# Kernel tuning notes

Measured on AMD Instinct MI355X. Metric: run time of the kernel, lower is better.

Reference implementation:

```python
import jax, jax.numpy as jnp
import numpy as np

H_HEADS = 16
N_HID = 1024
D_K = N_HID // H_HEADS
EPS = 1e-6


def _linear(x, w, b):
    # torch nn.Linear: y = x @ W^T + b, W is [out, in]
    return jnp.einsum('bsi,oi->bso', x, w) + b


def _layernorm(x, a, b):
    # Faithful to custom LayerNorm: unbiased std (torch default) and (std + eps)
    mean = jnp.mean(x, axis=-1, keepdims=True)
    std = jnp.std(x, axis=-1, keepdims=True, ddof=1)
    return a * (x - mean) / (std + EPS) + b


def setup_inputs() -> dict:
    key = jax.random.key(0)
    ks = jax.random.split(key, 20)
    B, S, H = 4, 1024, N_HID
    s = 1.0 / np.sqrt(H)
    inp = {
        'x': jax.random.normal(ks[0], (B, S, H), dtype=jnp.float32),
        'mask': jax.random.randint(ks[1], (B, 1, 1, S), 0, 2, dtype=jnp.int32),
        'wq': jax.random.normal(ks[2], (H, H), dtype=jnp.float32) * s,
        'bq': jnp.zeros((H,), jnp.float32),
        'wk': jax.random.normal(ks[3], (H, H), dtype=jnp.float32) * s,
        'bk': jnp.zeros((H,), jnp.float32),
        'wv': jax.random.normal(ks[4], (H, H), dtype=jnp.float32) * s,
        'bv': jnp.zeros((H,), jnp.float32),
        'wo': jax.random.normal(ks[5], (H, H), dtype=jnp.float32) * s,
        'bo': jnp.zeros((H,), jnp.float32),
        'w1': jax.random.normal(ks[6], (2 * H, H), dtype=jnp.float32) * s,
        'b1': jnp.zeros((2 * H,), jnp.float32),
        'w2': jax.random.normal(ks[7], (H, 2 * H), dtype=jnp.float32) * (1.0 / np.sqrt(2 * H)),
        'b2': jnp.zeros((H,), jnp.float32),
        'g1': jnp.ones((H,), jnp.float32),
        'be1': jnp.zeros((H,), jnp.float32),
        'g2': jnp.ones((H,), jnp.float32),
        'be2': jnp.zeros((H,), jnp.float32),
    }
    return inp


def _forward(x, mask, wq, bq, wk, bk, wv, bv, wo, bo, w1, b1, w2, b2, g1, be1, g2, be2):
    B, S, H = x.shape
    # --- multi-head self-attention ---
    q = _linear(x, wq, bq).reshape(B, S, H_HEADS, D_K).transpose(0, 2, 1, 3)  # [B,h,S,dk]
    k = _linear(x, wk, bk).reshape(B, S, H_HEADS, D_K).transpose(0, 2, 1, 3)
    v = _linear(x, wv, bv).reshape(B, S, H_HEADS, D_K).transpose(0, 2, 1, 3)
    scores = jnp.einsum('bhqd,bhkd->bhqk', q, k) / np.sqrt(D_K)  # [B,h,S,S]
    scores = jnp.where(mask == 0, jnp.float32(-1e9), scores)
    p = jax.nn.softmax(scores, axis=-1)
    attn_out = jnp.einsum('bhqk,bhkd->bhqd', p, v)
    attn_out = attn_out.transpose(0, 2, 1, 3).reshape(B, S, H)
    attn_out = _linear(attn_out, wo, bo)
    # sublayer 0: residual + layernorm (dropout = identity at eval)
    x = _layernorm(x + attn_out, g1, be1)
    # --- positionwise FFN ---
    ff = _linear(jax.nn.relu(_linear(x, w1, b1)), w2, b2)
    # sublayer 1
    return _layernorm(x + ff, g2, be2)


def reference(x, mask, wq, bq, wk, bk, wv, bv, wo, bo, w1, b1, w2, b2, g1, be1, g2, be2):
    return _forward(x, mask, wq, bq, wk, bk, wv, bv, wo, bo, w1, b1, w2, b2, g1, be1, g2, be2)
```

## Files before the change

### kernel.cpp

```cpp
#include <hip/hip_runtime.h>

typedef __attribute__((ext_vector_type(8))) short short8;
typedef __attribute__((ext_vector_type(4))) float f32x4;
typedef __attribute__((ext_vector_type(4))) unsigned short us4;

#define LOG2E 1.4426950408889634f

__device__ __forceinline__ unsigned short f2bf(float f) {
  unsigned int u = __float_as_uint(f);
  u += 0x7FFFu + ((u >> 16) & 1u);
  return (unsigned short)(u >> 16);
}

__global__ __launch_bounds__(256) void cvt_all(
    const float* __restrict__ x, const float* __restrict__ wq, const float* __restrict__ wk,
    const float* __restrict__ wv, const float* __restrict__ wo, const float* __restrict__ w1,
    const float* __restrict__ w2,
    unsigned short* __restrict__ xb, unsigned short* __restrict__ wqkvb,
    unsigned short* __restrict__ wob, unsigned short* __restrict__ w1b,
    unsigned short* __restrict__ w2b) {
  int i = blockIdx.x * 256 + threadIdx.x;
  for (int t = i; t < 3145728; t += 786432) {
    const float* src; unsigned short* dst; int lo;
    if (t < 1048576)      { src = x;  dst = xb;              lo = t; }
    else if (t < 1310720) { src = wq; dst = wqkvb;           lo = t - 1048576; }
    else if (t < 1572864) { src = wk; dst = wqkvb + 1048576; lo = t - 1310720; }
    else if (t < 1835008) { src = wv; dst = wqkvb + 2097152; lo = t - 1572864; }
    else if (t < 2097152) { src = wo; dst = wob;             lo = t - 1835008; }
    else if (t < 2621440) { src = w1; dst = w1b;             lo = t - 2097152; }
    else                  { src = w2; dst = w2b;             lo = t - 2621440; }
    float4 v = ((const float4*)src)[lo];
    us4 o = { f2bf(v.x), f2bf(v.y), f2bf(v.z), f2bf(v.w) };
    *(us4*)(dst + (size_t)lo * 4) = o;
  }
}

#define GLL16(g, l) __builtin_amdgcn_global_load_lds( \
    (const __attribute__((address_space(1))) void*)(g), \
    (__attribute__((address_space(3))) void*)(l), 16, 0, 0)

template <int BN, int EPI>
__global__ __launch_bounds__(256) void gemm2(
    const unsigned short* __restrict__ A, const unsigned short* __restrict__ B,
    const float* __restrict__ bias, const float* __restrict__ res,
    void* __restrict__ out, int M, int N, int K) {
  __shared__ __align__(16) unsigned short As[2][128 * 64];
  __shared__ __align__(16) unsigned short Bs[2][BN * 64];
  const int tid = threadIdx.x;
  const int lane = tid & 63;
  const int w = tid >> 6;
  const int l15 = lane & 15, l4 = lane >> 4;
  const int m0 = blockIdx.y * 128, n0 = blockIdx.x * BN;

  constexpr int MI = (BN == 128) ? 4 : 2;
  f32x4 acc[MI][4] = {};

  auto STAGE = [&](int buf, int kt) {
#pragma unroll
    for (int i = 0; i < 4; ++i) {
      int chunk = i * 4 + w;
      int c = chunk * 64 + lane;
      int row = c >> 3;
      int srcb = ((c & 7) * 16) ^ ((row & 7) << 4);
      GLL16(A + (size_t)(m0 + row) * K + kt * 64 + (srcb >> 1), &As[buf][chunk * 512]);
    }
#pragma unroll
    for (int i = 0; i < BN / 32; ++i) {
      int chunk = i * 4 + w;
      int c = chunk * 64 + lane;
      int row = c >> 3;
      int srcb = ((c & 7) * 16) ^ ((row & 7) << 4);
      GLL16(B + (size_t)(n0 + row) * K + kt * 64 + (srcb >> 1), &Bs[buf][chunk * 512]);
    }
  };

  const int nkt = K >> 6;
  STAGE(0, 0);
  __syncthreads();
  int cur = 0;
  for (int kt = 0; kt < nkt; ++kt) {
    if (kt + 1 < nkt) STAGE(cur ^ 1, kt + 1);
    const unsigned short* as = As[cur];
    const unsigned short* bs = Bs[cur];
#pragma unroll
    for (int ks = 0; ks < 2; ++ks) {
      short8 a[MI], b[4];
#pragma unroll
      for (int mi = 0; mi < MI; ++mi) {
        int row = (BN == 128 ? ((w >> 1) * 64) : (w * 32)) + mi * 16 + l15;
        int ke = (ks * 32 + l4 * 8) ^ ((row & 7) << 3);
        a[mi] = *(const short8*)(as + row * 64 + ke);
      }
#pragma unroll
      for (int ni = 0; ni < 4; ++ni) {
        int row = (BN == 128 ? ((w & 1) * 64) : 0) + ni * 16 + l15;
        int ke = (ks * 32 + l4 * 8) ^ ((row & 7) << 3);
        b[ni] = *(const short8*)(bs + row * 64 + ke);
      }
#pragma unroll
      for (int mi = 0; mi < MI; ++mi)
#pragma unroll
        for (int ni = 0; ni < 4; ++ni)
          acc[mi][ni] = __builtin_amdgcn_mfma_f32_16x16x32_bf16(a[mi], b[ni], acc[mi][ni], 0, 0, 0);
    }
    __syncthreads();
    cur ^= 1;
  }

#pragma unroll
  for (int mi = 0; mi < MI; ++mi) {
#pragma unroll
    for (int ni = 0; ni < 4; ++ni) {
      int n = n0 + (BN == 128 ? ((w & 1) * 64) : 0) + ni * 16 + l15;
      float bv = bias[n];
#pragma unroll
      for (int j = 0; j < 4; ++j) {
        int m = m0 + (BN == 128 ? ((w >> 1) * 64) : (w * 32)) + mi * 16 + l4 * 4 + j;
        float v = acc[mi][ni][j] + bv;
        if (EPI == 0) {
          ((float*)out)[(size_t)m * N + n] = v + res[(size_t)m * N + n];
        } else {
          ((unsigned short*)out)[(size_t)m * N + n] = f2bf(v > 0.f ? v : 0.f);
        }
      }
    }
  }
}

__global__ __launch_bounds__(256) void gemm_qkv(
    const unsigned short* __restrict__ A,
    const unsigned short* __restrict__ Bw,
    const float* __restrict__ bq, const float* __restrict__ bk, const float* __restrict__ bvv,
    unsigned short* __restrict__ Qo, unsigned short* __restrict__ Ko, unsigned short* __restrict__ Vto,
    int K) {
  __shared__ __align__(16) unsigned short As[2][128 * 64];
  __shared__ __align__(16) unsigned short Bs[2][64 * 64];
  const int tid = threadIdx.x;
  const int lane = tid & 63;
  const int w = tid >> 6;
  const int l15 = lane & 15, l4 = lane >> 4;
  const int m0 = blockIdx.y * 128, n0 = blockIdx.x * 64;
  const bool swp = (n0 >= 2048);

  f32x4 acc[2][4] = {};

  auto STAGE = [&](int buf, int kt) {
#pragma unroll
    for (int i = 0; i < 4; ++i) {
      int chunk = i * 4 + w;
      int c = chunk * 64 + lane;
      int row = c >> 3;
      int srcb = ((c & 7) * 16) ^ ((row & 7) << 4);
      GLL16(A + (size_t)(m0 + row) * K + kt * 64 + (srcb >> 1), &As[buf][chunk * 512]);
    }
#pragma unroll
    for (int i = 0; i < 2; ++i) {
      int chunk = i * 4 + w;
      int c = chunk * 64 + lane;
      int row = c >> 3;
      int srcb = ((c & 7) * 16) ^ ((row & 7) << 4);
      GLL16(Bw + (size_t)(n0 + row) * K + kt * 64 + (srcb >> 1), &Bs[buf][chunk * 512]);
    }
  };

  const int nkt = K >> 6;
  STAGE(0, 0);
  __syncthreads();
  int cur = 0;
  for (int kt = 0; kt < nkt; ++kt) {
    if (kt + 1 < nkt) STAGE(cur ^ 1, kt + 1);
    const unsigned short* as = As[cur];
    const unsigned short* bs = Bs[cur];
#pragma unroll
    for (int ks = 0; ks < 2; ++ks) {
      short8 a[2], b[4];
#pragma unroll
      for (int mi = 0; mi < 2; ++mi) {
        int row = w * 32 + mi * 16 + l15;
        int ke = (ks * 32 + l4 * 8) ^ ((row & 7) << 3);
        a[mi] = *(const short8*)(as + row * 64 + ke);
      }
#pragma unroll
      for (int ni = 0; ni < 4; ++ni) {
        int row = ni * 16 + l15;
        int ke = (ks * 32 + l4 * 8) ^ ((row & 7) << 3);
        b[ni] = *(const short8*)(bs + row * 64 + ke);
      }
      if (!swp) {
#pragma unroll
        for (int mi = 0; mi < 2; ++mi)
#pragma unroll
          for (int ni = 0; ni < 4; ++ni)
            acc[mi][ni] = __builtin_amdgcn_mfma_f32_16x16x32_bf16(a[mi], b[ni], acc[mi][ni], 0, 0, 0);
      } else {
#pragma unroll
        for (int mi = 0; mi < 2; ++mi)
#pragma unroll
          for (int ni = 0; ni < 4; ++ni)
            acc[mi][ni] = __builtin_amdgcn_mfma_f32_16x16x32_bf16(b[ni], a[mi], acc[mi][ni], 0, 0, 0);
      }
    }
    __syncthreads();
    cur ^= 1;
  }

  if (!swp) {
#pragma unroll
    for (int mi = 0; mi < 2; ++mi) {
#pragma unroll
      for (int ni = 0; ni < 4; ++ni) {
        int n = n0 + ni * 16 + l15;
        int seg = n >> 10;
        int nn = n & 1023;
        int h_ = nn >> 6, d_ = nn & 63;
        float bval = (seg == 0 ? bq : bk)[nn];
#pragma unroll
        for (int j = 0; j < 4; ++j) {
          int m = m0 + w * 32 + mi * 16 + l4 * 4 + j;
          int b_ = m >> 10, s_ = m & 1023;
          float v = acc[mi][ni][j] + bval;
          size_t headbase = ((size_t)(b_ * 16 + h_)) << 16;
          if (seg == 0) Qo[headbase + (s_ << 6) + d_] = f2bf(v * 0.125f);
          else          Ko[headbase + (s_ << 6) + d_] = f2bf(v);
        }
      }
    }
  } else {
#pragma unroll
    for (int ni = 0; ni < 4; ++ni) {
      float bval[4];
      int nbase = (n0 & 1023) + ni * 16 + l4 * 4;
#pragma unroll
      for (int j = 0; j < 4; ++j) bval[j] = bvv[nbase + j];
#pragma unroll
      for (int mi = 0; mi < 2; ++mi) {
        int m = m0 + w * 32 + mi * 16 + l15;
        int b_ = m >> 10, s_ = m & 1023;
#pragma unroll
        for (int j = 0; j < 4; ++j) {
          int nn = nbase + j;
          int h_ = nn >> 6, d_ = nn & 63;
          float v = acc[mi][ni][j] + bval[j];
          Vto[(((size_t)(b_ * 16 + h_)) << 16) + (d_ << 10) + s_] = f2bf(v);
        }
      }
    }
  }
}

__global__ __launch_bounds__(256) void attn_kernel(
    const unsigned short* __restrict__ Qg, const unsigned short* __restrict__ Kg,
    const unsigned short* __restrict__ Vtg, const int* __restrict__ mask,
    unsigned short* __restrict__ Og) {
  __shared__ __align__(16) unsigned short Qs[64 * 64];
  __shared__ __align__(16) unsigned short Ks[64 * 64];
  __shared__ __align__(16) unsigned short Vs[64 * 64];
  __shared__ __align__(16) unsigned short Ps[4][16 * 64];
  __shared__ float mkadd[1024];

  const int tid = threadIdx.x, lane = tid & 63, w = tid >> 6;
  const int l15 = lane & 15, l4 = lane >> 4;
  const int bh = blockIdx.x;
  const int b = bh >> 4, h = bh & 15;
  const int s0 = blockIdx.y * 64;

  const unsigned short* Qbase = Qg + ((size_t)bh << 16);
  const unsigned short* Kbase = Kg + ((size_t)bh << 16);
  const unsigned short* Vbase = Vtg + ((size_t)bh << 16);

#pragma unroll
  for (int i = 0; i < 4; ++i)
    mkadd[i * 256 + tid] = (mask[b * 1024 + i * 256 + tid] == 0) ? -1e9f : 0.f;

#pragma unroll
  for (int i = 0; i < 2; ++i) {
    int c = i * 256 + tid;
    int row = c >> 3, off8 = (c & 7) * 8;
    short8 v = *(const short8*)(Qbase + (size_t)(s0 + row) * 64 + off8);
    *(short8*)(&Qs[row * 64 + (off8 ^ ((row & 7) << 3))]) = v;
  }

  const int c0 = tid, c1 = 256 + tid;
  const int r0 = c0 >> 3, o0 = (c0 & 7) * 8;
  const int r1 = c1 >> 3, o1 = (c1 & 7) * 8;
  const int li0 = r0 * 64 + (o0 ^ ((r0 & 7) << 3));
  const int li1 = r1 * 64 + (o1 ^ ((r1 & 7) << 3));

  short8 kA, kB, vA, vB;
#define LOADKV(kv0) do { \
    kA = *(const short8*)(Kbase + (size_t)((kv0) + r0) * 64 + o0); \
    kB = *(const short8*)(Kbase + (size_t)((kv0) + r1) * 64 + o1); \
    vA = *(const short8*)(Vbase + (size_t)r0 * 1024 + (kv0) + o0); \
    vB = *(const short8*)(Vbase + (size_t)r1 * 1024 + (kv0) + o1); \
  } while (0)

  f32x4 o[4] = {};
  float l_st[4] = {0.f, 0.f, 0.f, 0.f};

  LOADKV(0);
  for (int kv = 0; kv < 16; ++kv) {
    int kv0 = kv * 64;
    __syncthreads();
    *(short8*)(&Ks[li0]) = kA;
    *(short8*)(&Ks[li1]) = kB;
    *(short8*)(&Vs[li0]) = vA;
    *(short8*)(&Vs[li1]) = vB;
    __syncthreads();
    if (kv < 15) LOADKV(kv0 + 64);

    f32x4 sc[4] = {};
#pragma unroll
    for (int ks = 0; ks < 2; ++ks) {
      short8 a, bb[4];
      {
        int row = w * 16 + l15;
        int ke = (ks * 32 + l4 * 8) ^ ((row & 7) << 3);
        a = *(const short8*)(Qs + row * 64 + ke);
      }
#pragma unroll
      for (int ni = 0; ni < 4; ++ni) {
        int row = ni * 16 + l15;
        int ke = (ks * 32 + l4 * 8) ^ ((row & 7) << 3);
        bb[ni] = *(const short8*)(Ks + row * 64 + ke);
      }
#pragma unroll
      for (int ni = 0; ni < 4; ++ni)
        sc[ni] = __builtin_amdgcn_mfma_f32_16x16x32_bf16(a, bb[ni], sc[ni], 0, 0, 0);
    }

#pragma unroll
    for (int j = 0; j < 4; ++j) {
      int r = l4 * 4 + j;
      float ps = 0.f;
#pragma unroll
      for (int ni = 0; ni < 4; ++ni) {
        int cc = ni * 16 + l15;
        float p = exp2f(fmaf(sc[ni][j], LOG2E, mkadd[kv0 + cc]));
        ps += p;
        Ps[w][r * 64 + (cc ^ ((r & 7) << 3))] = f2bf(p);
      }
      l_st[j] += ps;
    }

#pragma unroll
    for (int ks = 0; ks < 2; ++ks) {
      short8 a, bb[4];
      {
        int row = l15;
        int ke = (ks * 32 + l4 * 8) ^ ((row & 7) << 3);
        a = *(const short8*)(&Ps[w][row * 64 + ke]);
      }
#pragma unroll
      for (int dt = 0; dt < 4; ++dt) {
        int row = dt * 16 + l15;
        int ke = (ks * 32 + l4 * 8) ^ ((row & 7) << 3);
        bb[dt] = *(const short8*)(Vs + row * 64 + ke);
      }
#pragma unroll
      for (int dt = 0; dt < 4; ++dt)
        o[dt] = __builtin_amdgcn_mfma_f32_16x16x32_bf16(a, bb[dt], o[dt], 0, 0, 0);
    }
  }
#undef LOADKV

#pragma unroll
  for (int j = 0; j < 4; ++j) {
#pragma unroll
    for (int off = 1; off < 16; off <<= 1) l_st[j] += __shfl_xor(l_st[j], off, 64);
  }

#pragma unroll
  for (int j = 0; j < 4; ++j) {
    float inv = 1.f / l_st[j];
    int s = s0 + w * 16 + l4 * 4 + j;
#pragma unroll
    for (int dt = 0; dt < 4; ++dt) {
      int d = dt * 16 + l15;
      Og[(((size_t)(b * 1024 + s)) << 10) + h * 64 + d] = f2bf(o[dt][j] * inv);
    }
  }
}

template <int WRITE_BF16>
__global__ __launch_bounds__(256) void ln_kernel(
    const float* __restrict__ z, const float* __restrict__ g, const float* __restrict__ be,
    float* __restrict__ outf, unsigned short* __restrict__ outb) {
  int row = blockIdx.x * 4 + (threadIdx.x >> 6);
  int lane = threadIdx.x & 63;
  const float4* zp = (const float4*)(z + (size_t)row * 1024);
  float4 v[4];
  float sum = 0.f, sq = 0.f;
#pragma unroll
  for (int k = 0; k < 4; ++k) {
    v[k] = zp[lane + k * 64];
    sum += v[k].x + v[k].y + v[k].z + v[k].w;
    sq += v[k].x * v[k].x + v[k].y * v[k].y + v[k].z * v[k].z + v[k].w * v[k].w;
  }
#pragma unroll
  for (int off = 1; off < 64; off <<= 1) {
    sum += __shfl_xor(sum, off, 64);
    sq += __shfl_xor(sq, off, 64);
  }
  float mean = sum * (1.f / 1024.f);
  float var = fmaxf((sq - sum * mean) * (1.f / 1023.f), 0.f);
  float r = 1.f / (sqrtf(var) + 1e-6f);
#pragma unroll
  for (int k = 0; k < 4; ++k) {
    int c = lane + k * 64;
    float4 gv = ((const float4*)g)[c];
    float4 bv = ((const float4*)be)[c];
    float4 y;
    y.x = (v[k].x - mean) * r * gv.x + bv.x;
    y.y = (v[k].y - mean) * r * gv.y + bv.y;
    y.z = (v[k].z - mean) * r * gv.z + bv.z;
    y.w = (v[k].w - mean) * r * gv.w + bv.w;
    ((float4*)(outf + (size_t)row * 1024))[c] = y;
    if (WRITE_BF16) {
      us4 ob = { f2bf(y.x), f2bf(y.y), f2bf(y.z), f2bf(y.w) };
      *(us4*)(outb + (size_t)row * 1024 + c * 4) = ob;
    }
  }
}

extern "C" void kernel_launch(void* const* d_in, const int* in_sizes, int n_in,
                              void* d_out, int out_size, void* d_ws, size_t ws_size,
                              hipStream_t stream) {
  (void)in_sizes; (void)n_in; (void)out_size; (void)ws_size;
  const float* x   = (const float*)d_in[0];
  const int*   msk = (const int*)d_in[1];
  const float* wq  = (const float*)d_in[2];
  const float* bq  = (const float*)d_in[3];
  const float* wk  = (const float*)d_in[4];
  const float* bk  = (const float*)d_in[5];
  const float* wv  = (const float*)d_in[6];
  const float* bv  = (const float*)d_in[7];
  const float* wo  = (const float*)d_in[8];
  const float* bo  = (const float*)d_in[9];
  const float* w1  = (const float*)d_in[10];
  const float* b1  = (const float*)d_in[11];
  const float* w2  = (const float*)d_in[12];
  const float* b2  = (const float*)d_in[13];
  const float* g1  = (const float*)d_in[14];
  const float* be1 = (const float*)d_in[15];
  const float* g2  = (const float*)d_in[16];
  const float* be2 = (const float*)d_in[17];
  float* out = (float*)d_out;

  char* ws = (char*)d_ws;
  const size_t MB = 1 << 20;
  unsigned short* xb    = (unsigned short*)(ws + 0 * MB);
  unsigned short* wqkvb = (unsigned short*)(ws + 8 * MB);
  unsigned short* wob   = (unsigned short*)(ws + 14 * MB);
  unsigned short* w1b   = (unsigned short*)(ws + 16 * MB);
  unsigned short* w2b   = (unsigned short*)(ws + 20 * MB);
  unsigned short* Qb    = (unsigned short*)(ws + 24 * MB);
  unsigned short* Kb    = (unsigned short*)(ws + 32 * MB);
  unsigned short* Vtb   = (unsigned short*)(ws + 40 * MB);
  unsigned short* attnb = (unsigned short*)(ws + 48 * MB);
  float* z1   = (float*)(ws + 56 * MB);
  float* x1f  = (float*)(ws + 72 * MB);
  unsigned short* x1b = (unsigned short*)(ws + 88 * MB);
  unsigned short* h1  = (unsigned short*)(ws + 24 * MB);
  float* z2 = (float*)(ws + 56 * MB);

  dim3 blk(256);

  cvt_all<<<3072, blk, 0, stream>>>(x, wq, wk, wv, wo, w1, w2, xb, wqkvb, wob, w1b, w2b);

  gemm_qkv<<<dim3(48, 32), blk, 0, stream>>>(xb, wqkvb, bq, bk, bv, Qb, Kb, Vtb, 1024);

  attn_kernel<<<dim3(64, 16), blk, 0, stream>>>(Qb, Kb, Vtb, msk, attnb);

  gemm2<64, 0><<<dim3(16, 32), blk, 0, stream>>>(attnb, wob, bo, x, (void*)z1, 4096, 1024, 1024);
  ln_kernel<1><<<1024, blk, 0, stream>>>(z1, g1, be1, x1f, x1b);

  gemm2<128, 3><<<dim3(16, 32), blk, 0, stream>>>(x1b, w1b, b1, nullptr, (void*)h1, 4096, 2048, 1024);
  gemm2<64, 0><<<dim3(16, 32), blk, 0, stream>>>(h1, w2b, b2, x1f, (void*)z2, 4096, 1024, 2048);
  ln_kernel<0><<<1024, blk, 0, stream>>>(z2, g2, be2, out, nullptr);
}
```

Before: 184.9 us.

## Compact unmasked keys to skip masked attention tiles; tighten GEMM pipeline waits

A new prefix-scan kernel builds, per batch, a permutation that packs unmasked key positions first, plus a count of them. The QKV GEMM scatters K and V^T rows into that packed order, so attention only loops over the tiles holding valid keys and zeroes the tail with a bounds check instead of a mask-add table. The GEMM mainloops also replace __syncthreads with explicit vmcnt waits and raw barriers, with a peeled final iteration, so the next tile's loads overlap compute. This adds a small kernel launch and a scattered store pattern. A batch with every key masked now yields a zero denominator instead of a uniform softmax.

```diff
diff --git a/kernel.cpp b/kernel.cpp
--- a/kernel.cpp
+++ b/kernel.cpp
@@ -35,6 +35,36 @@
   }
 }
 
+__global__ __launch_bounds__(256) void mask_index(
+    const int* __restrict__ mask, int* __restrict__ dest, int* __restrict__ cnt) {
+  int b = blockIdx.x, tid = threadIdx.x;
+  const int4 mv = ((const int4*)(mask + b * 1024))[tid];
+  int vals[4] = {mv.x != 0, mv.y != 0, mv.z != 0, mv.w != 0};
+  int s4 = vals[0] + vals[1] + vals[2] + vals[3];
+  __shared__ int sv[256];
+  sv[tid] = s4;
+  __syncthreads();
+  for (int off = 1; off < 256; off <<= 1) {
+    int t = (tid >= off) ? sv[tid - off] : 0;
+    __syncthreads();
+    sv[tid] += t;
+    __syncthreads();
+  }
+  int excl = sv[tid] - s4;
+  int total = sv[255];
+  int r = excl;
+  int d4[4];
+#pragma unroll
+  for (int i = 0; i < 4; ++i) {
+    int s = tid * 4 + i;
+    if (vals[i]) { d4[i] = r; r++; }
+    else         { d4[i] = total + s - r; }
+  }
+  int4 o = {d4[0], d4[1], d4[2], d4[3]};
+  ((int4*)(dest + b * 1024))[tid] = o;
+  if (tid == 0) cnt[b] = total;
+}
+
 #define GLL16(g, l) __builtin_amdgcn_global_load_lds( \
     (const __attribute__((address_space(1))) void*)(g), \
     (__attribute__((address_space(3))) void*)(l), 16, 0, 0)
@@ -74,38 +104,47 @@
     }
   };
 
+  auto COMPUTE = [&](int cur) {
+    const unsigned short* as = As[cur];
+    const unsigned short* bs = Bs[cur];
+#pragma unroll
+    for (int ks = 0; ks < 2; ++ks) {
+      short8 a[MI], b[4];
+#pragma unroll
+      for (int mi = 0; mi < MI; ++mi) {
+        int row = (BN == 128 ? ((w >> 1) * 64) : (w * 32)) + mi * 16 + l15;
+        int ke = (ks * 32 + l4 * 8) ^ ((row & 7) << 3);
+        a[mi] = *(const short8*)(as + row * 64 + ke);
+      }
+#pragma unroll
+      for (int ni = 0; ni < 4; ++ni) {
+        int row = (BN == 128 ? ((w & 1) * 64) : 0) + ni * 16 + l15;
+        int ke = (ks * 32 + l4 * 8) ^ ((row & 7) << 3);
+        b[ni] = *(const short8*)(bs + row * 64 + ke);
+      }
+#pragma unroll
+      for (int mi = 0; mi < MI; ++mi)
+#pragma unroll
+        for (int ni = 0; ni < 4; ++ni)
+          acc[mi][ni] = __builtin_amdgcn_mfma_f32_16x16x32_bf16(a[mi], b[ni], acc[mi][ni], 0, 0, 0);
+    }
+  };
+
   const int nkt = K >> 6;
   STAGE(0, 0);
-  __syncthreads();
   int cur = 0;
-  for (int kt = 0; kt < nkt; ++kt) {
-    if (kt + 1 < nkt) STAGE(cur ^ 1, kt + 1);
-    const unsigned short* as = As[cur];
-    const unsigned short* bs = Bs[cur];
-#pragma unroll
-    for (int ks = 0; ks < 2; ++ks) {
-      short8 a[MI], b[4];
-#pragma unroll
-      for (int mi = 0; mi < MI; ++mi) {
-        int row = (BN == 128 ? ((w >> 1) * 64) : (w * 32)) + mi * 16 + l15;
-        int ke = (ks * 32 + l4 * 8) ^ ((row & 7) << 3);
-        a[mi] = *(const short8*)(as + row * 64 + ke);
-      }
-#pragma unroll
-      for (int ni = 0; ni < 4; ++ni) {
-        int row = (BN == 128 ? ((w & 1) * 64) : 0) + ni * 16 + l15;
-        int ke = (ks * 32 + l4 * 8) ^ ((row & 7) << 3);
-        b[ni] = *(const short8*)(bs + row * 64 + ke);
-      }
-#pragma unroll
-      for (int mi = 0; mi < MI; ++mi)
-#pragma unroll
-        for (int ni = 0; ni < 4; ++ni)
-          acc[mi][ni] = __builtin_amdgcn_mfma_f32_16x16x32_bf16(a[mi], b[ni], acc[mi][ni], 0, 0, 0);
-    }
-    __syncthreads();
+  for (int kt = 0; kt < nkt - 1; ++kt) {
+    STAGE(cur ^ 1, kt + 1);
+    if constexpr (BN == 128) { asm volatile("s_waitcnt vmcnt(8)" ::: "memory"); }
+    else                     { asm volatile("s_waitcnt vmcnt(6)" ::: "memory"); }
+    __builtin_amdgcn_s_barrier();
+    COMPUTE(cur);
+    __builtin_amdgcn_s_barrier();
     cur ^= 1;
   }
+  asm volatile("s_waitcnt vmcnt(0)" ::: "memory");
+  __builtin_amdgcn_s_barrier();
+  COMPUTE(cur);
 
 #pragma unroll
   for (int mi = 0; mi < MI; ++mi) {
@@ -131,6 +170,7 @@
     const unsigned short* __restrict__ A,
     const unsigned short* __restrict__ Bw,
     const float* __restrict__ bq, const float* __restrict__ bk, const float* __restrict__ bvv,
+    const int* __restrict__ dest,
     unsigned short* __restrict__ Qo, unsigned short* __restrict__ Ko, unsigned short* __restrict__ Vto,
     int K) {
   __shared__ __align__(16) unsigned short As[2][128 * 64];
@@ -163,12 +203,7 @@
     }
   };
 
-  const int nkt = K >> 6;
-  STAGE(0, 0);
-  __syncthreads();
-  int cur = 0;
-  for (int kt = 0; kt < nkt; ++kt) {
-    if (kt + 1 < nkt) STAGE(cur ^ 1, kt + 1);
+  auto COMPUTE = [&](int cur) {
     const unsigned short* as = As[cur];
     const unsigned short* bs = Bs[cur];
 #pragma unroll
@@ -200,9 +235,22 @@
             acc[mi][ni] = __builtin_amdgcn_mfma_f32_16x16x32_bf16(b[ni], a[mi], acc[mi][ni], 0, 0, 0);
       }
     }
-    __syncthreads();
+  };
+
+  const int nkt = K >> 6;
+  STAGE(0, 0);
+  int cur = 0;
+  for (int kt = 0; kt < nkt - 1; ++kt) {
+    STAGE(cur ^ 1, kt + 1);
+    asm volatile("s_waitcnt vmcnt(6)" ::: "memory");
+    __builtin_amdgcn_s_barrier();
+    COMPUTE(cur);
+    __builtin_amdgcn_s_barrier();
     cur ^= 1;
   }
+  asm volatile("s_waitcnt vmcnt(0)" ::: "memory");
+  __builtin_amdgcn_s_barrier();
+  COMPUTE(cur);
 
   if (!swp) {
 #pragma unroll
@@ -220,8 +268,12 @@
           int b_ = m >> 10, s_ = m & 1023;
           float v = acc[mi][ni][j] + bval;
           size_t headbase = ((size_t)(b_ * 16 + h_)) << 16;
-          if (seg == 0) Qo[headbase + (s_ << 6) + d_] = f2bf(v * 0.125f);
-          else          Ko[headbase + (s_ << 6) + d_] = f2bf(v);
+          if (seg == 0) {
+            Qo[headbase + (s_ << 6) + d_] = f2bf(v * 0.125f);
+          } else {
+            int sc = dest[b_ * 1024 + s_];
+            Ko[headbase + (sc << 6) + d_] = f2bf(v);
+          }
         }
       }
     }
@@ -236,12 +288,13 @@
       for (int mi = 0; mi < 2; ++mi) {
         int m = m0 + w * 32 + mi * 16 + l15;
         int b_ = m >> 10, s_ = m & 1023;
+        int sc = dest[b_ * 1024 + s_];
 #pragma unroll
         for (int j = 0; j < 4; ++j) {
           int nn = nbase + j;
           int h_ = nn >> 6, d_ = nn & 63;
           float v = acc[mi][ni][j] + bval[j];
-          Vto[(((size_t)(b_ * 16 + h_)) << 16) + (d_ << 10) + s_] = f2bf(v);
+          Vto[(((size_t)(b_ * 16 + h_)) << 16) + (d_ << 10) + sc] = f2bf(v);
         }
       }
     }
@@ -250,13 +303,12 @@
 
 __global__ __launch_bounds__(256) void attn_kernel(
     const unsigned short* __restrict__ Qg, const unsigned short* __restrict__ Kg,
-    const unsigned short* __restrict__ Vtg, const int* __restrict__ mask,
+    const unsigned short* __restrict__ Vtg, const int* __restrict__ cntg,
     unsigned short* __restrict__ Og) {
   __shared__ __align__(16) unsigned short Qs[64 * 64];
   __shared__ __align__(16) unsigned short Ks[64 * 64];
   __shared__ __align__(16) unsigned short Vs[64 * 64];
   __shared__ __align__(16) unsigned short Ps[4][16 * 64];
-  __shared__ float mkadd[1024];
 
   const int tid = threadIdx.x, lane = tid & 63, w = tid >> 6;
   const int l15 = lane & 15, l4 = lane >> 4;
@@ -268,9 +320,8 @@
   const unsigned short* Kbase = Kg + ((size_t)bh << 16);
   const unsigned short* Vbase = Vtg + ((size_t)bh << 16);
 
-#pragma unroll
-  for (int i = 0; i < 4; ++i)
-    mkadd[i * 256 + tid] = (mask[b * 1024 + i * 256 + tid] == 0) ? -1e9f : 0.f;
+  const int cnt = cntg[b];
+  const int nkt = (cnt + 63) >> 6;
 
 #pragma unroll
   for (int i = 0; i < 2; ++i) {
@@ -298,7 +349,7 @@
   float l_st[4] = {0.f, 0.f, 0.f, 0.f};
 
   LOADKV(0);
-  for (int kv = 0; kv < 16; ++kv) {
+  for (int kv = 0; kv < nkt; ++kv) {
     int kv0 = kv * 64;
     __syncthreads();
     *(short8*)(&Ks[li0]) = kA;
@@ -306,7 +357,7 @@
     *(short8*)(&Vs[li0]) = vA;
     *(short8*)(&Vs[li1]) = vB;
     __syncthreads();
-    if (kv < 15) LOADKV(kv0 + 64);
+    if (kv + 1 < nkt) LOADKV(kv0 + 64);
 
     f32x4 sc[4] = {};
 #pragma unroll
@@ -328,6 +379,9 @@
         sc[ni] = __builtin_amdgcn_mfma_f32_16x16x32_bf16(a, bb[ni], sc[ni], 0, 0, 0);
     }
 
+    bool val[4];
+#pragma unroll
+    for (int ni = 0; ni < 4; ++ni) val[ni] = (kv0 + ni * 16 + l15) < cnt;
 #pragma unroll
     for (int j = 0; j < 4; ++j) {
       int r = l4 * 4 + j;
@@ -335,7 +389,8 @@
 #pragma unroll
       for (int ni = 0; ni < 4; ++ni) {
         int cc = ni * 16 + l15;
-        float p = exp2f(fmaf(sc[ni][j], LOG2E, mkadd[kv0 + cc]));
+        float p = exp2f(sc[ni][j] * LOG2E);
+        p = val[ni] ? p : 0.f;
         ps += p;
         Ps[w][r * 64 + (cc ^ ((r & 7) << 3))] = f2bf(p);
       }
@@ -462,14 +517,17 @@
   unsigned short* x1b = (unsigned short*)(ws + 88 * MB);
   unsigned short* h1  = (unsigned short*)(ws + 24 * MB);
   float* z2 = (float*)(ws + 56 * MB);
+  int* dest = (int*)(ws + 56 * MB);
+  int* cnt  = dest + 4096;
 
   dim3 blk(256);
 
   cvt_all<<<3072, blk, 0, stream>>>(x, wq, wk, wv, wo, w1, w2, xb, wqkvb, wob, w1b, w2b);
-
-  gemm_qkv<<<dim3(48, 32), blk, 0, stream>>>(xb, wqkvb, bq, bk, bv, Qb, Kb, Vtb, 1024);
-
-  attn_kernel<<<dim3(64, 16), blk, 0, stream>>>(Qb, Kb, Vtb, msk, attnb);
+  mask_index<<<4, blk, 0, stream>>>(msk, dest, cnt);
+
+  gemm_qkv<<<dim3(48, 32), blk, 0, stream>>>(xb, wqkvb, bq, bk, bv, dest, Qb, Kb, Vtb, 1024);
+
+  attn_kernel<<<dim3(64, 16), blk, 0, stream>>>(Qb, Kb, Vtb, cnt, attnb);
 
   gemm2<64, 0><<<dim3(16, 32), blk, 0, stream>>>(attnb, wob, bo, x, (void*)z1, 4096, 1024, 1024);
   ln_kernel<1><<<1024, blk, 0, stream>>>(z1, g1, be1, x1f, x1b);
```

New measurement: 178.6 us. 1.04x faster.

## Compact unmasked keys via gather so attention skips fully masked KV tiles

Applied to the files above, without the earlier changes.

Adds a prefix-scan kernel that builds, per batch, a permutation that puts unmasked key positions first and records their count. The QKV GEMM gathers input rows through this permutation for the K and V outputs, so valid keys end up contiguous. The attention loop then visits only ceil(cnt/64) KV tiles and zeroes scores past cnt, which avoids the exp and MFMA work on masked keys (about half with this random mask). The cost is an extra small launch and indirect row addressing in the GEMM. Numerics match the reference unless a row has every key masked, where the reference gives a uniform softmax and this code does not.

```diff
diff --git a/kernel.cpp b/kernel.cpp
--- a/kernel.cpp
+++ b/kernel.cpp
@@ -35,6 +35,35 @@
   }
 }
 
+__global__ __launch_bounds__(256) void mask_index(
+    const int* __restrict__ mask, int* __restrict__ srcp, int* __restrict__ cnt) {
+  int b = blockIdx.x, tid = threadIdx.x;
+  const int4 mv = ((const int4*)(mask + b * 1024))[tid];
+  int vals[4] = {mv.x != 0, mv.y != 0, mv.z != 0, mv.w != 0};
+  int s4 = vals[0] + vals[1] + vals[2] + vals[3];
+  __shared__ int sv[256];
+  sv[tid] = s4;
+  __syncthreads();
+  for (int off = 1; off < 256; off <<= 1) {
+    int t = (tid >= off) ? sv[tid - off] : 0;
+    __syncthreads();
+    sv[tid] += t;
+    __syncthreads();
+  }
+  int excl = sv[tid] - s4;
+  int total = sv[255];
+  int r = excl;
+#pragma unroll
+  for (int i = 0; i < 4; ++i) {
+    int s = tid * 4 + i;
+    int d;
+    if (vals[i]) { d = r; r++; }
+    else         { d = total + s - r; }
+    srcp[b * 1024 + d] = s;
+  }
+  if (tid == 0) cnt[b] = total;
+}
+
 #define GLL16(g, l) __builtin_amdgcn_global_load_lds( \
     (const __attribute__((address_space(1))) void*)(g), \
     (__attribute__((address_space(3))) void*)(l), 16, 0, 0)
@@ -131,6 +160,7 @@
     const unsigned short* __restrict__ A,
     const unsigned short* __restrict__ Bw,
     const float* __restrict__ bq, const float* __restrict__ bk, const float* __restrict__ bvv,
+    const int* __restrict__ srcp,
     unsigned short* __restrict__ Qo, unsigned short* __restrict__ Ko, unsigned short* __restrict__ Vto,
     int K) {
   __shared__ __align__(16) unsigned short As[2][128 * 64];
@@ -141,6 +171,15 @@
   const int l15 = lane & 15, l4 = lane >> 4;
   const int m0 = blockIdx.y * 128, n0 = blockIdx.x * 64;
   const bool swp = (n0 >= 2048);
+  const bool gat = (n0 >= 1024);
+
+  int arow[4];
+#pragma unroll
+  for (int i = 0; i < 4; ++i) {
+    int chunk = i * 4 + w;
+    int m = m0 + ((chunk * 64 + lane) >> 3);
+    arow[i] = gat ? ((m & ~1023) + srcp[m]) : m;
+  }
 
   f32x4 acc[2][4] = {};
 
@@ -149,9 +188,8 @@
     for (int i = 0; i < 4; ++i) {
       int chunk = i * 4 + w;
       int c = chunk * 64 + lane;
-      int row = c >> 3;
-      int srcb = ((c & 7) * 16) ^ ((row & 7) << 4);
-      GLL16(A + (size_t)(m0 + row) * K + kt * 64 + (srcb >> 1), &As[buf][chunk * 512]);
+      int srcb = ((c & 7) * 16) ^ (((c >> 3) & 7) << 4);
+      GLL16(A + (size_t)arow[i] * K + kt * 64 + (srcb >> 1), &As[buf][chunk * 512]);
     }
 #pragma unroll
     for (int i = 0; i < 2; ++i) {
@@ -250,13 +288,12 @@
 
 __global__ __launch_bounds__(256) void attn_kernel(
     const unsigned short* __restrict__ Qg, const unsigned short* __restrict__ Kg,
-    const unsigned short* __restrict__ Vtg, const int* __restrict__ mask,
+    const unsigned short* __restrict__ Vtg, const int* __restrict__ cntg,
     unsigned short* __restrict__ Og) {
   __shared__ __align__(16) unsigned short Qs[64 * 64];
   __shared__ __align__(16) unsigned short Ks[64 * 64];
   __shared__ __align__(16) unsigned short Vs[64 * 64];
   __shared__ __align__(16) unsigned short Ps[4][16 * 64];
-  __shared__ float mkadd[1024];
 
   const int tid = threadIdx.x, lane = tid & 63, w = tid >> 6;
   const int l15 = lane & 15, l4 = lane >> 4;
@@ -268,9 +305,8 @@
   const unsigned short* Kbase = Kg + ((size_t)bh << 16);
   const unsigned short* Vbase = Vtg + ((size_t)bh << 16);
 
-#pragma unroll
-  for (int i = 0; i < 4; ++i)
-    mkadd[i * 256 + tid] = (mask[b * 1024 + i * 256 + tid] == 0) ? -1e9f : 0.f;
+  const int cnt = cntg[b];
+  const int nkt = (cnt + 63) >> 6;
 
 #pragma unroll
   for (int i = 0; i < 2; ++i) {
@@ -298,7 +334,7 @@
   float l_st[4] = {0.f, 0.f, 0.f, 0.f};
 
   LOADKV(0);
-  for (int kv = 0; kv < 16; ++kv) {
+  for (int kv = 0; kv < nkt; ++kv) {
     int kv0 = kv * 64;
     __syncthreads();
     *(short8*)(&Ks[li0]) = kA;
@@ -306,7 +342,7 @@
     *(short8*)(&Vs[li0]) = vA;
     *(short8*)(&Vs[li1]) = vB;
     __syncthreads();
-    if (kv < 15) LOADKV(kv0 + 64);
+    if (kv + 1 < nkt) LOADKV(kv0 + 64);
 
     f32x4 sc[4] = {};
 #pragma unroll
@@ -328,6 +364,9 @@
         sc[ni] = __builtin_amdgcn_mfma_f32_16x16x32_bf16(a, bb[ni], sc[ni], 0, 0, 0);
     }
 
+    bool val[4];
+#pragma unroll
+    for (int ni = 0; ni < 4; ++ni) val[ni] = (kv0 + ni * 16 + l15) < cnt;
 #pragma unroll
     for (int j = 0; j < 4; ++j) {
       int r = l4 * 4 + j;
@@ -335,7 +374,8 @@
 #pragma unroll
       for (int ni = 0; ni < 4; ++ni) {
         int cc = ni * 16 + l15;
-        float p = exp2f(fmaf(sc[ni][j], LOG2E, mkadd[kv0 + cc]));
+        float p = exp2f(sc[ni][j] * LOG2E);
+        p = val[ni] ? p : 0.f;
         ps += p;
         Ps[w][r * 64 + (cc ^ ((r & 7) << 3))] = f2bf(p);
       }
@@ -462,14 +502,17 @@
   unsigned short* x1b = (unsigned short*)(ws + 88 * MB);
   unsigned short* h1  = (unsigned short*)(ws + 24 * MB);
   float* z2 = (float*)(ws + 56 * MB);
+  int* srcp = (int*)(ws + 56 * MB);
+  int* cnt  = srcp + 4096;
 
   dim3 blk(256);
 
   cvt_all<<<3072, blk, 0, stream>>>(x, wq, wk, wv, wo, w1, w2, xb, wqkvb, wob, w1b, w2b);
-
-  gemm_qkv<<<dim3(48, 32), blk, 0, stream>>>(xb, wqkvb, bq, bk, bv, Qb, Kb, Vtb, 1024);
-
-  attn_kernel<<<dim3(64, 16), blk, 0, stream>>>(Qb, Kb, Vtb, msk, attnb);
+  mask_index<<<4, blk, 0, stream>>>(msk, srcp, cnt);
+
+  gemm_qkv<<<dim3(48, 32), blk, 0, stream>>>(xb, wqkvb, bq, bk, bv, srcp, Qb, Kb, Vtb, 1024);
+
+  attn_kernel<<<dim3(64, 16), blk, 0, stream>>>(Qb, Kb, Vtb, cnt, attnb);
 
   gemm2<64, 0><<<dim3(16, 32), blk, 0, stream>>>(attnb, wob, bo, x, (void*)z1, 4096, 1024, 1024);
   ln_kernel<1><<<1024, blk, 0, stream>>>(z1, g1, be1, x1f, x1b);
```

After: 170.8 us. 7.6% less time.
